# Kernel optimization log

Hardware: AMD Instinct MI355X
Metric: run time of the kernel (lower is better)

The kernel has to match this reference:

```python
import jax, jax.numpy as jnp
import numpy as np

N_NODES = 50000
N_EDGES = 800000
D = 128
AVG_D_LOG = 2.833  # log(avg_degree + 1)
EPS = 1e-5


def setup_inputs() -> dict:
    key = jax.random.key(0)
    ks = jax.random.split(key, 8)
    h = jax.random.normal(ks[0], (N_NODES, D), dtype=jnp.float32)
    e = jax.random.normal(ks[1], (N_EDGES, D), dtype=jnp.float32)
    snorm_n = jax.random.uniform(ks[2], (N_NODES, 1), dtype=jnp.float32)
    src = jax.random.randint(ks[3], (N_EDGES,), 0, N_NODES)
    dst = jax.random.randint(ks[4], (N_EDGES,), 0, N_NODES)
    W_pre = jax.random.normal(ks[5], (3 * D, D), dtype=jnp.float32) * 0.05
    b_pre = jnp.zeros((D,), dtype=jnp.float32)
    W_post = jax.random.normal(ks[6], (13 * D, D), dtype=jnp.float32) * 0.05
    b_post = jnp.zeros((D,), dtype=jnp.float32)
    return {"h": h, "e": e, "snorm_n": snorm_n, "src": src, "dst": dst,
            "W_pre": W_pre, "b_pre": b_pre, "W_post": W_post, "b_post": b_post}


def _pna_forward(h, e, snorm_n, src, dst, W_pre, b_pre, W_post, b_post):
    N = h.shape[0]
    # pretrans_edges: gather endpoint features + edge features, single Linear (pretrans_layers=1)
    z2 = jnp.concatenate([h[src], h[dst], e], axis=1)           # [E, 3D]
    m = z2 @ W_pre + b_pre                                        # [E, D] per-edge message

    # reduce: multi-aggregator mailbox reduce over dst (ragged neighborhoods)
    deg = jax.ops.segment_sum(jnp.ones((m.shape[0],), m.dtype), dst, num_segments=N)  # [N]
    deg_safe = jnp.maximum(deg, 1.0)[:, None]
    s = jax.ops.segment_sum(m, dst, num_segments=N)
    s2 = jax.ops.segment_sum(m * m, dst, num_segments=N)
    mean = s / deg_safe
    var = jax.nn.relu(s2 / deg_safe - mean * mean)
    std = jnp.sqrt(var + EPS)
    mx = jax.ops.segment_max(m, dst, num_segments=N)
    mn = jax.ops.segment_min(m, dst, num_segments=N)
    has = (deg > 0)[:, None]
    mx = jnp.where(has, mx, 0.0)
    mn = jnp.where(has, mn, 0.0)
    agg = jnp.concatenate([mean, mx, mn, std], axis=1)            # [N, 4D]

    # scalers: identity, amplification, attenuation
    log_d = jnp.log(deg[:, None] + 1.0)
    log_d_safe = jnp.log(deg_safe + 1.0)
    amp = agg * (log_d / AVG_D_LOG)
    att = agg * (AVG_D_LOG / log_d_safe)
    scaled = jnp.concatenate([agg, amp, att], axis=1)             # [N, 12D]
    scaled = jnp.where(has, scaled, 0.0)                          # DGL zero-fills zero-degree nodes

    # posttrans: cat original h, single Linear (posttrans_layers=1), then graph_norm
    h_cat = jnp.concatenate([h, scaled], axis=1)                  # [N, 13D]
    out = h_cat @ W_post + b_post                                 # [N, D]
    out = out * snorm_n                                           # graph_norm; dropout p=0 is identity
    return out


def reference(h, e, snorm_n, src, dst, W_pre, b_pre, W_post, b_post):
    return _pna_forward(h, e, snorm_n, src, dst, W_pre, b_pre, W_post, b_post)
```

## Files before the change

### kernel.cpp

```cpp
#include <hip/hip_runtime.h>
#include <math.h>

#define NNODES 50000
#define NEDGES 800000
#define AVGDLOG 2.833f
#define EPSF 1e-5f
#define TPB_E 8

typedef __attribute__((ext_vector_type(8))) short short8;
typedef __attribute__((ext_vector_type(4))) float f32x4;

__device__ __forceinline__ unsigned f2bf(float x) {
    unsigned u = __float_as_uint(x);
    return (u + 0x7FFFu + ((u >> 16) & 1u)) >> 16;
}
__device__ __forceinline__ float bf2f(unsigned lo16) {
    return __uint_as_float(lo16 << 16);
}
__device__ __forceinline__ void up8(uint4 v, float* f) {
    f[0] = bf2f(v.x & 0xffffu); f[1] = bf2f(v.x >> 16);
    f[2] = bf2f(v.y & 0xffffu); f[3] = bf2f(v.y >> 16);
    f[4] = bf2f(v.z & 0xffffu); f[5] = bf2f(v.z >> 16);
    f[6] = bf2f(v.w & 0xffffu); f[7] = bf2f(v.w >> 16);
}
__device__ __forceinline__ uint4 pk8(const float* f) {
    uint4 v;
    v.x = f2bf(f[0]) | (f2bf(f[1]) << 16);
    v.y = f2bf(f[2]) | (f2bf(f[3]) << 16);
    v.z = f2bf(f[4]) | (f2bf(f[5]) << 16);
    v.w = f2bf(f[6]) | (f2bf(f[7]) << 16);
    return v;
}

__global__ void k_zero(unsigned* __restrict__ deg) {
    int i = blockIdx.x * 256 + threadIdx.x;
    if (i < NNODES) deg[i] = 0u;
}
__global__ void k_count(const int* __restrict__ dst, unsigned* __restrict__ deg) {
    int i = blockIdx.x * 256 + threadIdx.x;
    if (i < NEDGES) atomicAdd(&deg[dst[i]], 1u);
}
__global__ __launch_bounds__(1024) void k_scan(const unsigned* __restrict__ deg,
                                               int* __restrict__ base, int* __restrict__ cursor) {
    __shared__ int ps[1024];
    const int t = threadIdx.x;
    const int lo = t * 52;
    int s = 0;
    if (lo + 52 <= NNODES) {
        const int4* dp = (const int4*)(deg + lo);
#pragma unroll
        for (int i = 0; i < 13; ++i) { int4 v = dp[i]; s += v.x + v.y + v.z + v.w; }
    } else {
        for (int i = lo; i < NNODES; ++i) s += (int)deg[i];
    }
    ps[t] = s;
    __syncthreads();
    for (int off = 1; off < 1024; off <<= 1) {
        int v = (t >= off) ? ps[t - off] : 0;
        __syncthreads();
        ps[t] += v;
        __syncthreads();
    }
    int run = (t > 0) ? ps[t - 1] : 0;
    if (lo + 52 <= NNODES) {
        const int4* dp = (const int4*)(deg + lo);
        int4* bp = (int4*)(base + lo);
        int4* cp = (int4*)(cursor + lo);
#pragma unroll
        for (int i = 0; i < 13; ++i) {
            int4 v = dp[i]; int4 b;
            b.x = run; run += v.x; b.y = run; run += v.y;
            b.z = run; run += v.z; b.w = run; run += v.w;
            bp[i] = b; cp[i] = b;
        }
    } else {
        for (int i = lo; i < NNODES; ++i) { base[i] = run; cursor[i] = run; run += (int)deg[i]; }
    }
    if (t == 1023) base[NNODES] = run;
}
__global__ void k_scatter(const int* __restrict__ dst, const int* __restrict__ src,
                          int* __restrict__ cursor, int* __restrict__ sorted,
                          int* __restrict__ ssrc) {
    int i = blockIdx.x * 256 + threadIdx.x;
    if (i < NEDGES) {
        int d = dst[i];
        int slot = atomicAdd(&cursor[d], 1);
        sorted[slot] = i;
        ssrc[slot] = src[i];
    }
}

__global__ void k_convW(const float* __restrict__ Wpre, const float* __restrict__ Wpost,
                        unsigned short* __restrict__ W3t, unsigned short* __restrict__ W12t,
                        unsigned short* __restrict__ Bhat) {
    int i = blockIdx.x * 256 + threadIdx.x;
    if (i < 128 * 128) {
        int n = i & 127, k = i >> 7;
        W3t[n * 128 + k] = (unsigned short)f2bf(Wpre[(256 + k) * 128 + n]);
    }
    if (i < 256 * 128) {
        int n = i >> 7, k = i & 127;
        float v = (n < 128) ? Wpre[k * 128 + n] : Wpre[(128 + k) * 128 + (n - 128)];
        W12t[n * 128 + k] = (unsigned short)f2bf(v);
    }
    if (i < 640 * 384) {
        int kc = i / (384 * 32);
        int rem = i % (384 * 32);
        int n = rem >> 5, kk = rem & 31;
        int k = kc * 32 + kk, c = n & 127, g = n >> 7;
        float v;
        if (g == 0) v = Wpost[k * 128 + c];
        else if (g == 1) v = (k < 128) ? 0.f : Wpost[(512 + k) * 128 + c];
        else v = (k < 128) ? 0.f : Wpost[(1024 + k) * 128 + c];
        Bhat[i] = (unsigned short)f2bf(v);
    }
}

__global__ __launch_bounds__(256) void k_p12(const float* __restrict__ h,
                                             const unsigned short* __restrict__ W12t,
                                             unsigned short* __restrict__ P1,
                                             unsigned short* __restrict__ P2,
                                             unsigned short* __restrict__ Abuf) {
    __shared__ __align__(16) unsigned short As[64 * 128];
    __shared__ __align__(16) unsigned short Bs[256 * 128];
    const int t = threadIdx.x;
    const size_t row0 = (size_t)blockIdx.x * 64;
#pragma unroll
    for (int j = 0; j < 16; ++j) {
        int idx = t + 256 * j;
        int n = idx >> 4, q = idx & 15;
        uint4 wv = *(const uint4*)(W12t + n * 128 + q * 8);
        *(uint4*)((char*)Bs + n * 256 + ((q * 16) ^ ((n & 7) << 4))) = wv;
    }
#pragma unroll
    for (int j = 0; j < 8; ++j) {
        int idx = t + 256 * j;
        int r = idx >> 5, q = idx & 31;
        size_t row = row0 + r;
        uint2 p = {0u, 0u};
        if (row < NNODES) {
            float4 z = ((const float4*)h)[row * 32 + q];
            p.x = f2bf(z.x) | (f2bf(z.y) << 16);
            p.y = f2bf(z.z) | (f2bf(z.w) << 16);
            *(uint2*)(Abuf + row * 640 + q * 4) = p;
        }
        *(uint2*)((char*)As + r * 256 + ((q * 8) ^ ((r & 7) << 4))) = p;
    }
    __syncthreads();
    const int w = t >> 6, lane = t & 63, lrow = lane & 15, lkb = lane >> 4;
    f32x4 acc[16];
#pragma unroll
    for (int i = 0; i < 16; ++i) acc[i] = (f32x4){0.f, 0.f, 0.f, 0.f};
    const char* Abase = (const char*)As + (w * 16 + lrow) * 256;
    const unsigned aswz = (unsigned)(((w * 16 + lrow) & 7) << 4);
#pragma unroll
    for (int kk = 0; kk < 4; ++kk) {
        int kbyte = (kk * 32 + lkb * 8) * 2;
        short8 af = *(const short8*)(Abase + (kbyte ^ aswz));
#pragma unroll
        for (int nt = 0; nt < 16; ++nt) {
            int n = nt * 16 + lrow;
            short8 bf = *(const short8*)((const char*)Bs + n * 256 + (kbyte ^ ((n & 7) << 4)));
            acc[nt] = __builtin_amdgcn_mfma_f32_16x16x32_bf16(af, bf, acc[nt], 0, 0, 0);
        }
    }
#pragma unroll
    for (int half = 0; half < 2; ++half) {
        __syncthreads();
#pragma unroll
        for (int nt = 0; nt < 8; ++nt) {
            int c = nt * 16 + lrow;
#pragma unroll
            for (int i = 0; i < 4; ++i) {
                int lr = w * 16 + lkb * 4 + i;
                *(unsigned short*)((char*)As + lr * 256 + ((c * 2) ^ ((lr & 7) << 4))) =
                    (unsigned short)f2bf(acc[half * 8 + nt][i]);
            }
        }
        __syncthreads();
        unsigned short* dstP = half ? P2 : P1;
#pragma unroll
        for (int j = 0; j < 4; ++j) {
            int idx = t + 256 * j;
            int r = idx >> 4, q = idx & 15;
            size_t row = row0 + r;
            if (row < NNODES) {
                uint4 v = *(const uint4*)((const char*)As + r * 256 + ((q * 16) ^ ((r & 7) << 4)));
                *(uint4*)(dstP + row * 128 + q * 8) = v;
            }
        }
    }
}

__global__ __launch_bounds__(256) void k_gemm_e(const float* __restrict__ e,
                                                const int* __restrict__ sorted,
                                                const unsigned short* __restrict__ W3t,
                                                const float* __restrict__ bpre,
                                                unsigned short* __restrict__ G) {
    __shared__ __align__(16) unsigned short Bs[128 * 128];
    __shared__ __align__(16) unsigned short As[2][64 * 128];
    __shared__ int Seid[TPB_E * 64];
    const int t = threadIdx.x;
    const int tile0 = blockIdx.x * TPB_E;
    const int ntiles = min(TPB_E, 12500 - tile0);

    for (int j = t; j < TPB_E * 64; j += 256) {
        int slot = tile0 * 64 + j;
        Seid[j] = (slot < NEDGES) ? sorted[slot] : 0;
    }
    __syncthreads();

    const int q = t & 31, r5 = t >> 5;
    auto loadE = [&](int ti, float4* ra) {
#pragma unroll
        for (int j = 0; j < 8; ++j) {
            int r = r5 + 8 * j;
            int eid = Seid[ti * 64 + r];
            ra[j] = ((const float4*)e)[(size_t)eid * 32 + q];
        }
    };
    auto storeA = [&](int buf, const float4* ra) {
#pragma unroll
        for (int j = 0; j < 8; ++j) {
            int r = r5 + 8 * j;
            uint2 pv;
            pv.x = f2bf(ra[j].x) | (f2bf(ra[j].y) << 16);
            pv.y = f2bf(ra[j].z) | (f2bf(ra[j].w) << 16);
            *(uint2*)((char*)As[buf] + r * 256 + ((q * 8) ^ ((r & 7) << 4))) = pv;
        }
    };

    float4 ra[8];
    loadE(0, ra);
#pragma unroll
    for (int j = 0; j < 8; ++j) {
        int idx = t + 256 * j;
        int n = idx >> 4, qq = idx & 15;
        uint4 wv = *(const uint4*)(W3t + n * 128 + qq * 8);
        *(uint4*)((char*)Bs + n * 256 + ((qq * 16) ^ ((n & 7) << 4))) = wv;
    }
    storeA(0, ra);
    if (ntiles > 1) loadE(1, ra);
    __syncthreads();

    const int w = t >> 6, lane = t & 63, lrow = lane & 15, lkb = lane >> 4;
    float bpf[8];
#pragma unroll
    for (int nt = 0; nt < 8; ++nt) bpf[nt] = bpre[nt * 16 + lrow];

    for (int ti = 0; ti < ntiles; ++ti) {
        const int c = ti & 1;
        f32x4 acc[8];
#pragma unroll
        for (int i = 0; i < 8; ++i) acc[i] = (f32x4){0.f, 0.f, 0.f, 0.f};
        const char* Ab = (const char*)As[c] + (w * 16 + lrow) * 256;
        const unsigned aswz = (unsigned)(((w * 16 + lrow) & 7) << 4);
#pragma unroll
        for (int kk = 0; kk < 4; ++kk) {
            int kbyte = (kk * 32 + lkb * 8) * 2;
            short8 af = *(const short8*)(Ab + (kbyte ^ aswz));
#pragma unroll
            for (int nt = 0; nt < 8; ++nt) {
                int n = nt * 16 + lrow;
                short8 bf = *(const short8*)((const char*)Bs + n * 256 + (kbyte ^ ((n & 7) << 4)));
                acc[nt] = __builtin_amdgcn_mfma_f32_16x16x32_bf16(af, bf, acc[nt], 0, 0, 0);
            }
        }
        __syncthreads();
#pragma unroll
        for (int nt = 0; nt < 8; ++nt) {
            int cc = nt * 16 + lrow;
#pragma unroll
            for (int i = 0; i < 4; ++i) {
                int lr = w * 16 + lkb * 4 + i;
                *(unsigned short*)((char*)As[c] + lr * 256 + ((cc * 2) ^ ((lr & 7) << 4))) =
                    (unsigned short)f2bf(acc[nt][i] + bpf[nt]);
            }
        }
        if (ti + 1 < ntiles) {
            storeA(c ^ 1, ra);
            if (ti + 2 < ntiles) loadE(ti + 2, ra);
        }
        __syncthreads();
        const size_t row0 = (size_t)(tile0 + ti) * 64;
#pragma unroll
        for (int j = 0; j < 4; ++j) {
            int idx = t + 256 * j;
            int r = idx >> 4, qq = idx & 15;
            uint4 v = *(const uint4*)((const char*)As[c] + r * 256 + ((qq * 16) ^ ((r & 7) << 4)));
            *(uint4*)(G + (row0 + r) * 128 + qq * 8) = v;
        }
    }
}

__global__ __launch_bounds__(256) void k_reduce(const unsigned short* __restrict__ G,
                                                const unsigned short* __restrict__ P1,
                                                const unsigned short* __restrict__ P2,
                                                const int* __restrict__ basep,
                                                const int* __restrict__ ssrc,
                                                unsigned short* __restrict__ Abuf) {
    const int t = threadIdx.x;
    const int n = blockIdx.x * 4 + (t >> 6);
    const int lane = t & 63, lq = lane >> 4, lc = lane & 15;
    int b0 = basep[n], b1 = basep[n + 1];
    int dg = b1 - b0;
    float s[8], q2[8], mx[8], mn[8];
#pragma unroll
    for (int j = 0; j < 8; ++j) { s[j] = 0.f; q2[j] = 0.f; mx[j] = -3.4e38f; mn[j] = 3.4e38f; }
    if (dg > 0) {
        float p2f[8];
        up8(*(const uint4*)(P2 + (size_t)n * 128 + lc * 8), p2f);
        for (int sl = b0 + lq; sl < b1; sl += 4) {
            int es = ssrc[sl];
            float gf[8], p1f[8];
            up8(*(const uint4*)(G + (size_t)sl * 128 + lc * 8), gf);
            up8(*(const uint4*)(P1 + (size_t)es * 128 + lc * 8), p1f);
#pragma unroll
            for (int j = 0; j < 8; ++j) {
                float m = gf[j] + p1f[j] + p2f[j];
                s[j] += m; q2[j] += m * m;
                mx[j] = fmaxf(mx[j], m); mn[j] = fminf(mn[j], m);
            }
        }
    }
#pragma unroll
    for (int off = 16; off <= 32; off <<= 1) {
#pragma unroll
        for (int j = 0; j < 8; ++j) {
            s[j] += __shfl_xor(s[j], off);
            q2[j] += __shfl_xor(q2[j], off);
            mx[j] = fmaxf(mx[j], __shfl_xor(mx[j], off));
            mn[j] = fminf(mn[j], __shfl_xor(mn[j], off));
        }
    }
    if (lane < 16) {
        float mean[8], sd[8], X[8], N[8];
        if (dg > 0) {
            float ds = (float)dg;
#pragma unroll
            for (int j = 0; j < 8; ++j) {
                mean[j] = s[j] / ds;
                float v = fmaxf(q2[j] / ds - mean[j] * mean[j], 0.f);
                sd[j] = sqrtf(v + EPSF);
                X[j] = mx[j]; N[j] = mn[j];
            }
        } else {
#pragma unroll
            for (int j = 0; j < 8; ++j) { mean[j] = 0.f; sd[j] = 0.f; X[j] = 0.f; N[j] = 0.f; }
        }
        unsigned short* row = Abuf + (size_t)n * 640 + 128 + lc * 8;
        *(uint4*)(row) = pk8(mean);
        *(uint4*)(row + 128) = pk8(X);
        *(uint4*)(row + 256) = pk8(N);
        *(uint4*)(row + 384) = pk8(sd);
    }
}

__global__ __launch_bounds__(512) void k_gemm_post(const unsigned short* __restrict__ Abuf,
                                                   const unsigned short* __restrict__ Bhat,
                                                   const float* __restrict__ bpost,
                                                   const float* __restrict__ snorm,
                                                   const int* __restrict__ basep,
                                                   float* __restrict__ out) {
    __shared__ __align__(16) unsigned short As[2][128 * 32];
    __shared__ __align__(16) unsigned short Bs[2][384 * 32];
    __shared__ float sAmp[128], sAtt[128], sSn[128], sBp[128];
    const int t = threadIdx.x;
    const size_t row0 = (size_t)blockIdx.x * 128;
    if (t < 128) {
        size_t nn = row0 + t;
        float a = 0.f, b = 0.f, sn = 0.f;
        if (nn < NNODES) {
            int dgi = basep[nn + 1] - basep[nn];
            a = logf((float)dgi + 1.f) * (1.f / AVGDLOG);
            b = AVGDLOG / logf(fmaxf((float)dgi, 1.f) + 1.f);
            sn = snorm[nn];
        }
        sAmp[t] = a; sAtt[t] = b; sSn[t] = sn; sBp[t] = bpost[t];
    }
    const int arow = t >> 2, ak4 = t & 3;
    auto loadA = [&](int kc, uint4& ra) {
        ra = (uint4){0u, 0u, 0u, 0u};
        if (row0 + arow < NNODES)
            ra = *(const uint4*)(Abuf + (row0 + arow) * 640 + kc * 32 + ak4 * 8);
    };
    auto loadB = [&](int kc, uint4* rb) {
#pragma unroll
        for (int j = 0; j < 3; ++j) {
            int idx = t + 512 * j;
            int n = idx >> 2, k4 = idx & 3;
            rb[j] = *(const uint4*)(Bhat + ((size_t)kc * 384 + n) * 32 + k4 * 8);
        }
    };
    auto storeLDS = [&](int buf, const uint4& ra, const uint4* rb) {
        *(uint4*)((char*)As[buf] + arow * 64 + ((ak4 * 16) ^ (((arow >> 1) & 3) << 4))) = ra;
#pragma unroll
        for (int j = 0; j < 3; ++j) {
            int idx = t + 512 * j;
            int n = idx >> 2, k4 = idx & 3;
            *(uint4*)((char*)Bs[buf] + n * 64 + ((k4 * 16) ^ (((n >> 1) & 3) << 4))) = rb[j];
        }
    };
    const int w = t >> 6, wm = w & 1, wn = w >> 1;
    const int lane = t & 63, lrow = lane & 15, lkb = lane >> 4;
    f32x4 acc[4][6];
#pragma unroll
    for (int a = 0; a < 4; ++a)
#pragma unroll
        for (int b = 0; b < 6; ++b) acc[a][b] = (f32x4){0.f, 0.f, 0.f, 0.f};

    uint4 ra, rb[3];
    loadA(0, ra); loadB(0, rb);
    storeLDS(0, ra, rb);
    int cur = 0;
    for (int kc = 0; kc < 20; ++kc) {
        if (kc < 19) { loadA(kc + 1, ra); loadB(kc + 1, rb); }
        __syncthreads();
        short8 af[4];
#pragma unroll
        for (int mi = 0; mi < 4; ++mi) {
            int r = wm * 64 + mi * 16 + lrow;
            af[mi] = *(const short8*)((const char*)As[cur] + r * 64 + ((lkb * 16) ^ (((r >> 1) & 3) << 4)));
        }
        short8 bfv[6];
#pragma unroll
        for (int g = 0; g < 3; ++g)
#pragma unroll
            for (int j = 0; j < 2; ++j) {
                int nn = g * 128 + wn * 32 + j * 16 + lrow;
                bfv[g * 2 + j] = *(const short8*)((const char*)Bs[cur] + nn * 64 + ((lkb * 16) ^ (((nn >> 1) & 3) << 4)));
            }
#pragma unroll
        for (int mi = 0; mi < 4; ++mi)
#pragma unroll
            for (int f = 0; f < 6; ++f)
                acc[mi][f] = __builtin_amdgcn_mfma_f32_16x16x32_bf16(af[mi], bfv[f], acc[mi][f], 0, 0, 0);
        if (kc < 19) storeLDS(cur ^ 1, ra, rb);
        cur ^= 1;
    }
#pragma unroll
    for (int mi = 0; mi < 4; ++mi)
#pragma unroll
        for (int j = 0; j < 2; ++j)
#pragma unroll
            for (int i = 0; i < 4; ++i) {
                int r = wm * 64 + mi * 16 + lkb * 4 + i;
                size_t grow = row0 + r;
                if (grow < NNODES) {
                    int c = wn * 32 + j * 16 + lrow;
                    float v = acc[mi][j][i] + sAmp[r] * acc[mi][2 + j][i] + sAtt[r] * acc[mi][4 + j][i] + sBp[c];
                    out[grow * 128 + c] = v * sSn[r];
                }
            }
}

extern "C" void kernel_launch(void* const* d_in, const int* in_sizes, int n_in,
                              void* d_out, int out_size, void* d_ws, size_t ws_size,
                              hipStream_t stream) {
    const float* h = (const float*)d_in[0];
    const float* e = (const float*)d_in[1];
    const float* snorm = (const float*)d_in[2];
    const int* src = (const int*)d_in[3];
    const int* dst = (const int*)d_in[4];
    const float* Wpre = (const float*)d_in[5];
    const float* bpre = (const float*)d_in[6];
    const float* Wpost = (const float*)d_in[7];
    const float* bpost = (const float*)d_in[8];
    float* out = (float*)d_out;

    char* p = (char*)d_ws;
    auto alloc = [&](size_t bytes) { char* r = p; p += (bytes + 255) & ~(size_t)255; return r; };
    unsigned short* P1 = (unsigned short*)alloc((size_t)NNODES * 128 * 2);
    unsigned short* P2 = (unsigned short*)alloc((size_t)NNODES * 128 * 2);
    unsigned short* Abuf = (unsigned short*)alloc((size_t)NNODES * 640 * 2);
    unsigned short* G = (unsigned short*)alloc((size_t)NEDGES * 128 * 2);
    unsigned short* W3t = (unsigned short*)alloc(128 * 128 * 2);
    unsigned short* W12t = (unsigned short*)alloc(256 * 128 * 2);
    unsigned short* Bhat = (unsigned short*)alloc((size_t)640 * 384 * 2);
    unsigned* deg = (unsigned*)alloc((size_t)NNODES * 4);
    int* basep = (int*)alloc((size_t)(NNODES + 1) * 4);
    int* cursor = (int*)alloc((size_t)NNODES * 4);
    int* sorted = (int*)alloc((size_t)NEDGES * 4);
    int* ssrc = (int*)alloc((size_t)NEDGES * 4);

    k_zero<<<(NNODES + 255) / 256, 256, 0, stream>>>(deg);
    k_count<<<(NEDGES + 255) / 256, 256, 0, stream>>>(dst, deg);
    k_scan<<<1, 1024, 0, stream>>>(deg, basep, cursor);
    k_scatter<<<(NEDGES + 255) / 256, 256, 0, stream>>>(dst, src, cursor, sorted, ssrc);
    k_convW<<<(640 * 384 + 255) / 256, 256, 0, stream>>>(Wpre, Wpost, W3t, W12t, Bhat);
    k_p12<<<(NNODES + 63) / 64, 256, 0, stream>>>(h, W12t, P1, P2, Abuf);
    k_gemm_e<<<(12500 + TPB_E - 1) / TPB_E, 256, 0, stream>>>(e, sorted, W3t, bpre, G);
    k_reduce<<<NNODES / 4, 256, 0, stream>>>(G, P1, P2, basep, ssrc, Abuf);
    k_gemm_post<<<(NNODES + 127) / 128, 512, 0, stream>>>(Abuf, Bhat, bpost, snorm, basep, out);
}
```

Before: 479.3 us.

## Fuse edge GEMM with segmented multi-aggregator reduce over node-aligned edge chunks

Merges the per-edge pre-transform GEMM and the per-node mean/max/min/std reduction into one kernel. Each block takes a chunk of dst-sorted edges aligned to node boundaries, computes messages in shared memory and reduces them serially per column. This removes the 800K×128 bf16 intermediate message buffer round-trip through global memory. In exchange, the reduction is serial per tile using only 128 threads. Nodes with MAXS-bounded chunks or more than 32 zero-degree nodes per chunk may be mishandled, and the software pipeline is shallower.

```diff
diff --git a/kernel.cpp b/kernel.cpp
--- a/kernel.cpp
+++ b/kernel.cpp
@@ -5,7 +5,9 @@
 #define NEDGES 800000
 #define AVGDLOG 2.833f
 #define EPSF 1e-5f
-#define TPB_E 8
+#define CHUNK 448
+#define MAXS 576
+#define NCHUNK (NEDGES / CHUNK + 1)
 
 typedef __attribute__((ext_vector_type(8))) short short8;
 typedef __attribute__((ext_vector_type(4))) float f32x4;
@@ -16,20 +18,6 @@
 }
 __device__ __forceinline__ float bf2f(unsigned lo16) {
     return __uint_as_float(lo16 << 16);
-}
-__device__ __forceinline__ void up8(uint4 v, float* f) {
-    f[0] = bf2f(v.x & 0xffffu); f[1] = bf2f(v.x >> 16);
-    f[2] = bf2f(v.y & 0xffffu); f[3] = bf2f(v.y >> 16);
-    f[4] = bf2f(v.z & 0xffffu); f[5] = bf2f(v.z >> 16);
-    f[6] = bf2f(v.w & 0xffffu); f[7] = bf2f(v.w >> 16);
-}
-__device__ __forceinline__ uint4 pk8(const float* f) {
-    uint4 v;
-    v.x = f2bf(f[0]) | (f2bf(f[1]) << 16);
-    v.y = f2bf(f[2]) | (f2bf(f[3]) << 16);
-    v.z = f2bf(f[4]) | (f2bf(f[5]) << 16);
-    v.w = f2bf(f[6]) | (f2bf(f[7]) << 16);
-    return v;
 }
 
 __global__ void k_zero(unsigned* __restrict__ deg) {
@@ -192,68 +180,116 @@
     }
 }
 
-__global__ __launch_bounds__(256) void k_gemm_e(const float* __restrict__ e,
-                                                const int* __restrict__ sorted,
-                                                const unsigned short* __restrict__ W3t,
-                                                const float* __restrict__ bpre,
-                                                unsigned short* __restrict__ G) {
+__global__ __launch_bounds__(256) void k_fused(const float* __restrict__ e,
+                                               const int* __restrict__ sorted,
+                                               const int* __restrict__ ssrc_g,
+                                               const int* __restrict__ basep,
+                                               const unsigned short* __restrict__ W3t,
+                                               const float* __restrict__ bpre,
+                                               const unsigned short* __restrict__ P1,
+                                               const unsigned short* __restrict__ P2,
+                                               unsigned short* __restrict__ Abuf) {
     __shared__ __align__(16) unsigned short Bs[128 * 128];
-    __shared__ __align__(16) unsigned short As[2][64 * 128];
-    __shared__ int Seid[TPB_E * 64];
+    __shared__ __align__(16) unsigned short As[64 * 128];
+    __shared__ __align__(16) unsigned short P1s[64 * 128];
+    __shared__ int seid[MAXS];
+    __shared__ unsigned short ssr[MAXS];
+    __shared__ unsigned short snode[MAXS];
+    __shared__ int zlist[32];
+    __shared__ int zcnt;
+
     const int t = threadIdx.x;
-    const int tile0 = blockIdx.x * TPB_E;
-    const int ntiles = min(TPB_E, 12500 - tile0);
-
-    for (int j = t; j < TPB_E * 64; j += 256) {
-        int slot = tile0 * 64 + j;
-        Seid[j] = (slot < NEDGES) ? sorted[slot] : 0;
+    const int cblk = blockIdx.x;
+    if (t == 0) zcnt = 0;
+
+    const int tg1 = cblk * CHUNK, tg2 = tg1 + CHUNK;
+    int lo = 0, hi = NNODES;
+    while (lo < hi) { int mid = (lo + hi) >> 1; if (basep[mid] >= tg1) hi = mid; else lo = mid + 1; }
+    const int firstNode = lo;
+    hi = NNODES;
+    while (lo < hi) { int mid = (lo + hi) >> 1; if (basep[mid] >= tg2) hi = mid; else lo = mid + 1; }
+    const int endNode = lo;
+
+    const int s0 = basep[firstNode];
+    const int nslots = basep[endNode] - s0;
+    const int ntiles = (nslots + 63) >> 6;
+
+    const int ntot = ntiles << 6;
+    for (int j = t; j < ntot; j += 256) {
+        bool v = j < nslots;
+        seid[j] = v ? sorted[s0 + j] : 0;
+        ssr[j] = v ? (unsigned short)ssrc_g[s0 + j] : 0;
+    }
+    for (int n = firstNode + t; n < endNode; n += 256) {
+        int b0 = basep[n], b1 = basep[n + 1];
+        if (b0 == b1) { int i = atomicAdd(&zcnt, 1); if (i < 32) zlist[i] = n; }
+        for (int j = b0 - s0; j < b1 - s0; ++j) snode[j] = (unsigned short)n;
+    }
+#pragma unroll
+    for (int j = 0; j < 8; ++j) {
+        int idx = t + 256 * j;
+        int n = idx >> 4, q = idx & 15;
+        uint4 wv = *(const uint4*)(W3t + n * 128 + q * 8);
+        *(uint4*)((char*)Bs + n * 256 + ((q * 16) ^ ((n & 7) << 4))) = wv;
     }
     __syncthreads();
 
-    const int q = t & 31, r5 = t >> 5;
-    auto loadE = [&](int ti, float4* ra) {
+    const int q5 = t & 31, r5 = t >> 5;
+    float4 rE[8];
+    uint2 rP[8];
+    auto loadT = [&](int ti) {
 #pragma unroll
         for (int j = 0; j < 8; ++j) {
-            int r = r5 + 8 * j;
-            int eid = Seid[ti * 64 + r];
-            ra[j] = ((const float4*)e)[(size_t)eid * 32 + q];
-        }
-    };
-    auto storeA = [&](int buf, const float4* ra) {
+            int sl = (ti << 6) + r5 + 8 * j;
+            int eid = seid[sl];
+            rE[j] = ((const float4*)e)[(size_t)eid * 32 + q5];
+            int es = ssr[sl];
+            rP[j] = *(const uint2*)(P1 + (size_t)es * 128 + q5 * 4);
+        }
+    };
+    auto storeT = [&]() {
 #pragma unroll
         for (int j = 0; j < 8; ++j) {
             int r = r5 + 8 * j;
             uint2 pv;
-            pv.x = f2bf(ra[j].x) | (f2bf(ra[j].y) << 16);
-            pv.y = f2bf(ra[j].z) | (f2bf(ra[j].w) << 16);
-            *(uint2*)((char*)As[buf] + r * 256 + ((q * 8) ^ ((r & 7) << 4))) = pv;
-        }
-    };
-
-    float4 ra[8];
-    loadE(0, ra);
-#pragma unroll
-    for (int j = 0; j < 8; ++j) {
-        int idx = t + 256 * j;
-        int n = idx >> 4, qq = idx & 15;
-        uint4 wv = *(const uint4*)(W3t + n * 128 + qq * 8);
-        *(uint4*)((char*)Bs + n * 256 + ((qq * 16) ^ ((n & 7) << 4))) = wv;
-    }
-    storeA(0, ra);
-    if (ntiles > 1) loadE(1, ra);
-    __syncthreads();
+            pv.x = f2bf(rE[j].x) | (f2bf(rE[j].y) << 16);
+            pv.y = f2bf(rE[j].z) | (f2bf(rE[j].w) << 16);
+            unsigned off = (unsigned)(r * 256) + (((unsigned)(q5 * 8)) ^ (((unsigned)(r & 7)) << 4));
+            *(uint2*)((char*)As + off) = pv;
+            *(uint2*)((char*)P1s + off) = rP[j];
+        }
+    };
+    if (ntiles > 0) loadT(0);
 
     const int w = t >> 6, lane = t & 63, lrow = lane & 15, lkb = lane >> 4;
     float bpf[8];
 #pragma unroll
     for (int nt = 0; nt < 8; ++nt) bpf[nt] = bpre[nt * 16 + lrow];
 
+    const int col = t & 127;
+    float ss = 0.f, qq = 0.f, mx = -3.4e38f, mn = 3.4e38f;
+    int cur = -1;
+    auto flushN = [&]() {
+        float dg = (float)(basep[cur + 1] - basep[cur]);
+        float mean_g = ss / dg;
+        float var = fmaxf(qq / dg - mean_g * mean_g, 0.f);
+        float sd = sqrtf(var + EPSF);
+        float c2 = bf2f(P2[(size_t)cur * 128 + col]);
+        unsigned short* row = Abuf + (size_t)cur * 640 + 128 + col;
+        row[0] = (unsigned short)f2bf(mean_g + c2);
+        row[128] = (unsigned short)f2bf(mx + c2);
+        row[256] = (unsigned short)f2bf(mn + c2);
+        row[384] = (unsigned short)f2bf(sd);
+    };
+
     for (int ti = 0; ti < ntiles; ++ti) {
-        const int c = ti & 1;
+        storeT();
+        __syncthreads();
+        if (ti + 1 < ntiles) loadT(ti + 1);
         f32x4 acc[8];
 #pragma unroll
         for (int i = 0; i < 8; ++i) acc[i] = (f32x4){0.f, 0.f, 0.f, 0.f};
-        const char* Ab = (const char*)As[c] + (w * 16 + lrow) * 256;
+        const char* Ab = (const char*)As + (w * 16 + lrow) * 256;
         const unsigned aswz = (unsigned)(((w * 16 + lrow) & 7) << 4);
 #pragma unroll
         for (int kk = 0; kk < 4; ++kk) {
@@ -273,86 +309,36 @@
 #pragma unroll
             for (int i = 0; i < 4; ++i) {
                 int lr = w * 16 + lkb * 4 + i;
-                *(unsigned short*)((char*)As[c] + lr * 256 + ((cc * 2) ^ ((lr & 7) << 4))) =
-                    (unsigned short)f2bf(acc[nt][i] + bpf[nt]);
-            }
-        }
-        if (ti + 1 < ntiles) {
-            storeA(c ^ 1, ra);
-            if (ti + 2 < ntiles) loadE(ti + 2, ra);
-        }
-        __syncthreads();
-        const size_t row0 = (size_t)(tile0 + ti) * 64;
-#pragma unroll
-        for (int j = 0; j < 4; ++j) {
-            int idx = t + 256 * j;
-            int r = idx >> 4, qq = idx & 15;
-            uint4 v = *(const uint4*)((const char*)As[c] + r * 256 + ((qq * 16) ^ ((r & 7) << 4)));
-            *(uint4*)(G + (row0 + r) * 128 + qq * 8) = v;
-        }
-    }
-}
-
-__global__ __launch_bounds__(256) void k_reduce(const unsigned short* __restrict__ G,
-                                                const unsigned short* __restrict__ P1,
-                                                const unsigned short* __restrict__ P2,
-                                                const int* __restrict__ basep,
-                                                const int* __restrict__ ssrc,
-                                                unsigned short* __restrict__ Abuf) {
-    const int t = threadIdx.x;
-    const int n = blockIdx.x * 4 + (t >> 6);
-    const int lane = t & 63, lq = lane >> 4, lc = lane & 15;
-    int b0 = basep[n], b1 = basep[n + 1];
-    int dg = b1 - b0;
-    float s[8], q2[8], mx[8], mn[8];
-#pragma unroll
-    for (int j = 0; j < 8; ++j) { s[j] = 0.f; q2[j] = 0.f; mx[j] = -3.4e38f; mn[j] = 3.4e38f; }
-    if (dg > 0) {
-        float p2f[8];
-        up8(*(const uint4*)(P2 + (size_t)n * 128 + lc * 8), p2f);
-        for (int sl = b0 + lq; sl < b1; sl += 4) {
-            int es = ssrc[sl];
-            float gf[8], p1f[8];
-            up8(*(const uint4*)(G + (size_t)sl * 128 + lc * 8), gf);
-            up8(*(const uint4*)(P1 + (size_t)es * 128 + lc * 8), p1f);
-#pragma unroll
-            for (int j = 0; j < 8; ++j) {
-                float m = gf[j] + p1f[j] + p2f[j];
-                s[j] += m; q2[j] += m * m;
-                mx[j] = fmaxf(mx[j], m); mn[j] = fminf(mn[j], m);
-            }
-        }
-    }
-#pragma unroll
-    for (int off = 16; off <= 32; off <<= 1) {
-#pragma unroll
-        for (int j = 0; j < 8; ++j) {
-            s[j] += __shfl_xor(s[j], off);
-            q2[j] += __shfl_xor(q2[j], off);
-            mx[j] = fmaxf(mx[j], __shfl_xor(mx[j], off));
-            mn[j] = fminf(mn[j], __shfl_xor(mn[j], off));
-        }
-    }
-    if (lane < 16) {
-        float mean[8], sd[8], X[8], N[8];
-        if (dg > 0) {
-            float ds = (float)dg;
-#pragma unroll
-            for (int j = 0; j < 8; ++j) {
-                mean[j] = s[j] / ds;
-                float v = fmaxf(q2[j] / ds - mean[j] * mean[j], 0.f);
-                sd[j] = sqrtf(v + EPSF);
-                X[j] = mx[j]; N[j] = mn[j];
-            }
-        } else {
-#pragma unroll
-            for (int j = 0; j < 8; ++j) { mean[j] = 0.f; sd[j] = 0.f; X[j] = 0.f; N[j] = 0.f; }
-        }
-        unsigned short* row = Abuf + (size_t)n * 640 + 128 + lc * 8;
-        *(uint4*)(row) = pk8(mean);
-        *(uint4*)(row + 128) = pk8(X);
-        *(uint4*)(row + 256) = pk8(N);
-        *(uint4*)(row + 384) = pk8(sd);
+                unsigned off = (unsigned)(lr * 256) + (((unsigned)(cc * 2)) ^ (((unsigned)(lr & 7)) << 4));
+                float p1v = bf2f(*(const unsigned short*)((const char*)P1s + off));
+                *(unsigned short*)((char*)As + off) = (unsigned short)f2bf(acc[nt][i] + bpf[nt] + p1v);
+            }
+        }
+        __syncthreads();
+        const int rows = min(64, nslots - (ti << 6));
+        if (t < 128) {
+            for (int r = 0; r < rows; ++r) {
+                int n = (int)snode[(ti << 6) + r];
+                if (n != cur) {
+                    if (cur >= 0) flushN();
+                    cur = n; ss = 0.f; qq = 0.f; mx = -3.4e38f; mn = 3.4e38f;
+                }
+                unsigned off = (unsigned)(r * 256) + (((unsigned)(col * 2)) ^ (((unsigned)(r & 7)) << 4));
+                float x = bf2f(*(const unsigned short*)((const char*)As + off));
+                ss += x; qq = fmaf(x, x, qq);
+                mx = fmaxf(mx, x); mn = fminf(mn, x);
+            }
+        }
+        __syncthreads();
+    }
+    if (t < 128 && cur >= 0) flushN();
+    if (t < 128) {
+        int zc = min(zcnt, 32);
+        for (int i = 0; i < zc; ++i) {
+            int n = zlist[i];
+            unsigned short* row = Abuf + (size_t)n * 640 + 128 + col;
+            row[0] = 0; row[128] = 0; row[256] = 0; row[384] = 0;
+        }
     }
 }
 
@@ -473,7 +459,6 @@
     unsigned short* P1 = (unsigned short*)alloc((size_t)NNODES * 128 * 2);
     unsigned short* P2 = (unsigned short*)alloc((size_t)NNODES * 128 * 2);
     unsigned short* Abuf = (unsigned short*)alloc((size_t)NNODES * 640 * 2);
-    unsigned short* G = (unsigned short*)alloc((size_t)NEDGES * 128 * 2);
     unsigned short* W3t = (unsigned short*)alloc(128 * 128 * 2);
     unsigned short* W12t = (unsigned short*)alloc(256 * 128 * 2);
     unsigned short* Bhat = (unsigned short*)alloc((size_t)640 * 384 * 2);
@@ -489,7 +474,6 @@
     k_scatter<<<(NEDGES + 255) / 256, 256, 0, stream>>>(dst, src, cursor, sorted, ssrc);
     k_convW<<<(640 * 384 + 255) / 256, 256, 0, stream>>>(Wpre, Wpost, W3t, W12t, Bhat);
     k_p12<<<(NNODES + 63) / 64, 256, 0, stream>>>(h, W12t, P1, P2, Abuf);
-    k_gemm_e<<<(12500 + TPB_E - 1) / TPB_E, 256, 0, stream>>>(e, sorted, W3t, bpre, G);
-    k_reduce<<<NNODES / 4, 256, 0, stream>>>(G, P1, P2, basep, ssrc, Abuf);
+    k_fused<<<NCHUNK, 256, 0, stream>>>(e, sorted, ssrc, basep, W3t, bpre, P1, P2, Abuf);
     k_gemm_post<<<(NNODES + 127) / 128, 512, 0, stream>>>(Abuf, Bhat, bpost, snorm, basep, out);
 }
```

Result: slower. 576.6 us (+20.3%).

## Read edges in original order, scatter messages with P1 folded in, parallelize scan

Applied to the files above, without the earlier changes.

The edge GEMM now streams e contiguously and adds the gathered P1[src] term in its epilogue. It writes each message row to its dst-sorted slot, so the scatter pass only records slots and no longer builds sorted/ssrc arrays. The reduce loop reads only G and applies P2 after computing the statistics, using the shift invariance of mean/max/min/std. The single-block prefix scan is replaced by a three-kernel multi-block scan, and the LDS swizzle in the post GEMM is changed. In exchange, G writes become scattered rows and the P1 sum is rounded to bf16 before aggregation.

```diff
diff --git a/kernel.cpp b/kernel.cpp
--- a/kernel.cpp
+++ b/kernel.cpp
@@ -6,6 +6,7 @@
 #define AVGDLOG 2.833f
 #define EPSF 1e-5f
 #define TPB_E 8
+#define NSCAN 49
 
 typedef __attribute__((ext_vector_type(8))) short short8;
 typedef __attribute__((ext_vector_type(4))) float f32x4;
@@ -40,53 +41,67 @@
     int i = blockIdx.x * 256 + threadIdx.x;
     if (i < NEDGES) atomicAdd(&deg[dst[i]], 1u);
 }
-__global__ __launch_bounds__(1024) void k_scan(const unsigned* __restrict__ deg,
-                                               int* __restrict__ base, int* __restrict__ cursor) {
-    __shared__ int ps[1024];
-    const int t = threadIdx.x;
-    const int lo = t * 52;
+__global__ void k_scanA(const unsigned* __restrict__ deg, int* __restrict__ bsum) {
+    __shared__ int wsum[4];
+    const int t = threadIdx.x, b = blockIdx.x;
+    int i = b * 1024 + t * 4;
     int s = 0;
-    if (lo + 52 <= NNODES) {
-        const int4* dp = (const int4*)(deg + lo);
-#pragma unroll
-        for (int i = 0; i < 13; ++i) { int4 v = dp[i]; s += v.x + v.y + v.z + v.w; }
+    if (i + 4 <= NNODES) {
+        int4 v = *(const int4*)(deg + i);
+        s = v.x + v.y + v.z + v.w;
     } else {
-        for (int i = lo; i < NNODES; ++i) s += (int)deg[i];
-    }
-    ps[t] = s;
+        for (int k = 0; k < 4; ++k) if (i + k < NNODES) s += (int)deg[i + k];
+    }
+#pragma unroll
+    for (int off = 1; off < 64; off <<= 1) s += __shfl_xor(s, off);
+    if ((t & 63) == 0) wsum[t >> 6] = s;
     __syncthreads();
-    for (int off = 1; off < 1024; off <<= 1) {
-        int v = (t >= off) ? ps[t - off] : 0;
-        __syncthreads();
-        ps[t] += v;
-        __syncthreads();
-    }
-    int run = (t > 0) ? ps[t - 1] : 0;
-    if (lo + 52 <= NNODES) {
-        const int4* dp = (const int4*)(deg + lo);
-        int4* bp = (int4*)(base + lo);
-        int4* cp = (int4*)(cursor + lo);
-#pragma unroll
-        for (int i = 0; i < 13; ++i) {
-            int4 v = dp[i]; int4 b;
-            b.x = run; run += v.x; b.y = run; run += v.y;
-            b.z = run; run += v.z; b.w = run; run += v.w;
-            bp[i] = b; cp[i] = b;
-        }
+    if (t == 0) bsum[b] = wsum[0] + wsum[1] + wsum[2] + wsum[3];
+}
+__global__ void k_scanB(const int* __restrict__ bsum, int* __restrict__ boff,
+                        int* __restrict__ basep) {
+    if (threadIdx.x == 0) {
+        int run = 0;
+        for (int b = 0; b < NSCAN; ++b) { boff[b] = run; run += bsum[b]; }
+        basep[NNODES] = run;
+    }
+}
+__global__ void k_scanC(const unsigned* __restrict__ deg, const int* __restrict__ boff,
+                        int* __restrict__ basep, int* __restrict__ cursor) {
+    __shared__ int ps[256];
+    const int t = threadIdx.x, b = blockIdx.x;
+    int i = b * 1024 + t * 4;
+    int v0 = 0, v1 = 0, v2 = 0, v3 = 0;
+    if (i + 4 <= NNODES) {
+        int4 v = *(const int4*)(deg + i);
+        v0 = v.x; v1 = v.y; v2 = v.z; v3 = v.w;
     } else {
-        for (int i = lo; i < NNODES; ++i) { base[i] = run; cursor[i] = run; run += (int)deg[i]; }
-    }
-    if (t == 1023) base[NNODES] = run;
-}
-__global__ void k_scatter(const int* __restrict__ dst, const int* __restrict__ src,
-                          int* __restrict__ cursor, int* __restrict__ sorted,
-                          int* __restrict__ ssrc) {
+        if (i < NNODES) v0 = (int)deg[i];
+        if (i + 1 < NNODES) v1 = (int)deg[i + 1];
+        if (i + 2 < NNODES) v2 = (int)deg[i + 2];
+        if (i + 3 < NNODES) v3 = (int)deg[i + 3];
+    }
+    int ts = v0 + v1 + v2 + v3;
+    ps[t] = ts;
+    __syncthreads();
+    for (int off = 1; off < 256; off <<= 1) {
+        int x = (t >= off) ? ps[t - off] : 0;
+        __syncthreads();
+        ps[t] += x;
+        __syncthreads();
+    }
+    int excl = ps[t] - ts + boff[b];
+    if (i < NNODES) { basep[i] = excl; cursor[i] = excl; }
+    if (i + 1 < NNODES) { basep[i + 1] = excl + v0; cursor[i + 1] = excl + v0; }
+    if (i + 2 < NNODES) { basep[i + 2] = excl + v0 + v1; cursor[i + 2] = excl + v0 + v1; }
+    if (i + 3 < NNODES) { basep[i + 3] = excl + v0 + v1 + v2; cursor[i + 3] = excl + v0 + v1 + v2; }
+}
+__global__ void k_scatter(const int* __restrict__ dst, int* __restrict__ cursor,
+                          int* __restrict__ slotArr) {
     int i = blockIdx.x * 256 + threadIdx.x;
     if (i < NEDGES) {
         int d = dst[i];
-        int slot = atomicAdd(&cursor[d], 1);
-        sorted[slot] = i;
-        ssrc[slot] = src[i];
+        slotArr[i] = atomicAdd(&cursor[d], 1);
     }
 }
 
@@ -193,31 +208,32 @@
 }
 
 __global__ __launch_bounds__(256) void k_gemm_e(const float* __restrict__ e,
-                                                const int* __restrict__ sorted,
+                                                const int* __restrict__ src,
+                                                const int* __restrict__ slotArr,
                                                 const unsigned short* __restrict__ W3t,
                                                 const float* __restrict__ bpre,
+                                                const unsigned short* __restrict__ P1,
                                                 unsigned short* __restrict__ G) {
     __shared__ __align__(16) unsigned short Bs[128 * 128];
     __shared__ __align__(16) unsigned short As[2][64 * 128];
-    __shared__ int Seid[TPB_E * 64];
+    __shared__ int Ssl[TPB_E * 64];
+    __shared__ int Ssr[TPB_E * 64];
     const int t = threadIdx.x;
     const int tile0 = blockIdx.x * TPB_E;
     const int ntiles = min(TPB_E, 12500 - tile0);
 
-    for (int j = t; j < TPB_E * 64; j += 256) {
-        int slot = tile0 * 64 + j;
-        Seid[j] = (slot < NEDGES) ? sorted[slot] : 0;
-    }
-    __syncthreads();
+    for (int j = t; j < ntiles * 64; j += 256) {
+        int row = tile0 * 64 + j;
+        Ssl[j] = slotArr[row];
+        Ssr[j] = src[row];
+    }
 
     const int q = t & 31, r5 = t >> 5;
     auto loadE = [&](int ti, float4* ra) {
-#pragma unroll
-        for (int j = 0; j < 8; ++j) {
-            int r = r5 + 8 * j;
-            int eid = Seid[ti * 64 + r];
-            ra[j] = ((const float4*)e)[(size_t)eid * 32 + q];
-        }
+        const float4* ep = (const float4*)e + (size_t)(tile0 + ti) * 2048;
+#pragma unroll
+        for (int j = 0; j < 8; ++j)
+            ra[j] = ep[(r5 + 8 * j) * 32 + q];
     };
     auto storeA = [&](int buf, const float4* ra) {
 #pragma unroll
@@ -282,22 +298,24 @@
             if (ti + 2 < ntiles) loadE(ti + 2, ra);
         }
         __syncthreads();
-        const size_t row0 = (size_t)(tile0 + ti) * 64;
 #pragma unroll
         for (int j = 0; j < 4; ++j) {
             int idx = t + 256 * j;
             int r = idx >> 4, qq = idx & 15;
             uint4 v = *(const uint4*)((const char*)As[c] + r * 256 + ((qq * 16) ^ ((r & 7) << 4)));
-            *(uint4*)(G + (row0 + r) * 128 + qq * 8) = v;
+            uint4 pv = *(const uint4*)(P1 + (size_t)Ssr[ti * 64 + r] * 128 + qq * 8);
+            float gf[8], pf[8];
+            up8(v, gf); up8(pv, pf);
+#pragma unroll
+            for (int k = 0; k < 8; ++k) gf[k] += pf[k];
+            *(uint4*)(G + (size_t)Ssl[ti * 64 + r] * 128 + qq * 8) = pk8(gf);
         }
     }
 }
 
 __global__ __launch_bounds__(256) void k_reduce(const unsigned short* __restrict__ G,
-                                                const unsigned short* __restrict__ P1,
                                                 const unsigned short* __restrict__ P2,
                                                 const int* __restrict__ basep,
-                                                const int* __restrict__ ssrc,
                                                 unsigned short* __restrict__ Abuf) {
     const int t = threadIdx.x;
     const int n = blockIdx.x * 4 + (t >> 6);
@@ -307,20 +325,14 @@
     float s[8], q2[8], mx[8], mn[8];
 #pragma unroll
     for (int j = 0; j < 8; ++j) { s[j] = 0.f; q2[j] = 0.f; mx[j] = -3.4e38f; mn[j] = 3.4e38f; }
-    if (dg > 0) {
-        float p2f[8];
-        up8(*(const uint4*)(P2 + (size_t)n * 128 + lc * 8), p2f);
-        for (int sl = b0 + lq; sl < b1; sl += 4) {
-            int es = ssrc[sl];
-            float gf[8], p1f[8];
-            up8(*(const uint4*)(G + (size_t)sl * 128 + lc * 8), gf);
-            up8(*(const uint4*)(P1 + (size_t)es * 128 + lc * 8), p1f);
-#pragma unroll
-            for (int j = 0; j < 8; ++j) {
-                float m = gf[j] + p1f[j] + p2f[j];
-                s[j] += m; q2[j] += m * m;
-                mx[j] = fmaxf(mx[j], m); mn[j] = fminf(mn[j], m);
-            }
+    for (int sl = b0 + lq; sl < b1; sl += 4) {
+        float gf[8];
+        up8(*(const uint4*)(G + (size_t)sl * 128 + lc * 8), gf);
+#pragma unroll
+        for (int j = 0; j < 8; ++j) {
+            float m = gf[j];
+            s[j] += m; q2[j] = fmaf(m, m, q2[j]);
+            mx[j] = fmaxf(mx[j], m); mn[j] = fminf(mn[j], m);
         }
     }
 #pragma unroll
@@ -337,12 +349,16 @@
         float mean[8], sd[8], X[8], N[8];
         if (dg > 0) {
             float ds = (float)dg;
+            float p2f[8];
+            up8(*(const uint4*)(P2 + (size_t)n * 128 + lc * 8), p2f);
 #pragma unroll
             for (int j = 0; j < 8; ++j) {
-                mean[j] = s[j] / ds;
-                float v = fmaxf(q2[j] / ds - mean[j] * mean[j], 0.f);
+                float mg = s[j] / ds;
+                float v = fmaxf(q2[j] / ds - mg * mg, 0.f);
                 sd[j] = sqrtf(v + EPSF);
-                X[j] = mx[j]; N[j] = mn[j];
+                mean[j] = mg + p2f[j];
+                X[j] = mx[j] + p2f[j];
+                N[j] = mn[j] + p2f[j];
             }
         } else {
 #pragma unroll
@@ -393,12 +409,12 @@
         }
     };
     auto storeLDS = [&](int buf, const uint4& ra, const uint4* rb) {
-        *(uint4*)((char*)As[buf] + arow * 64 + ((ak4 * 16) ^ (((arow >> 1) & 3) << 4))) = ra;
+        *(uint4*)((char*)As[buf] + arow * 64 + ((ak4 * 16) ^ ((arow & 3) << 4))) = ra;
 #pragma unroll
         for (int j = 0; j < 3; ++j) {
             int idx = t + 512 * j;
             int n = idx >> 2, k4 = idx & 3;
-            *(uint4*)((char*)Bs[buf] + n * 64 + ((k4 * 16) ^ (((n >> 1) & 3) << 4))) = rb[j];
+            *(uint4*)((char*)Bs[buf] + n * 64 + ((k4 * 16) ^ ((n & 3) << 4))) = rb[j];
         }
     };
     const int w = t >> 6, wm = w & 1, wn = w >> 1;
@@ -420,7 +436,7 @@
 #pragma unroll
         for (int mi = 0; mi < 4; ++mi) {
             int r = wm * 64 + mi * 16 + lrow;
-            af[mi] = *(const short8*)((const char*)As[cur] + r * 64 + ((lkb * 16) ^ (((r >> 1) & 3) << 4)));
+            af[mi] = *(const short8*)((const char*)As[cur] + r * 64 + ((lkb * 16) ^ ((r & 3) << 4)));
         }
         short8 bfv[6];
 #pragma unroll
@@ -428,7 +444,7 @@
 #pragma unroll
             for (int j = 0; j < 2; ++j) {
                 int nn = g * 128 + wn * 32 + j * 16 + lrow;
-                bfv[g * 2 + j] = *(const short8*)((const char*)Bs[cur] + nn * 64 + ((lkb * 16) ^ (((nn >> 1) & 3) << 4)));
+                bfv[g * 2 + j] = *(const short8*)((const char*)Bs[cur] + nn * 64 + ((lkb * 16) ^ ((nn & 3) << 4)));
             }
 #pragma unroll
         for (int mi = 0; mi < 4; ++mi)
@@ -480,16 +496,19 @@
     unsigned* deg = (unsigned*)alloc((size_t)NNODES * 4);
     int* basep = (int*)alloc((size_t)(NNODES + 1) * 4);
     int* cursor = (int*)alloc((size_t)NNODES * 4);
-    int* sorted = (int*)alloc((size_t)NEDGES * 4);
-    int* ssrc = (int*)alloc((size_t)NEDGES * 4);
+    int* slotArr = (int*)alloc((size_t)NEDGES * 4);
+    int* bsum = (int*)alloc((size_t)NSCAN * 4);
+    int* boff = (int*)alloc((size_t)NSCAN * 4);
 
     k_zero<<<(NNODES + 255) / 256, 256, 0, stream>>>(deg);
     k_count<<<(NEDGES + 255) / 256, 256, 0, stream>>>(dst, deg);
-    k_scan<<<1, 1024, 0, stream>>>(deg, basep, cursor);
-    k_scatter<<<(NEDGES + 255) / 256, 256, 0, stream>>>(dst, src, cursor, sorted, ssrc);
+    k_scanA<<<NSCAN, 256, 0, stream>>>(deg, bsum);
+    k_scanB<<<1, 64, 0, stream>>>(bsum, boff, basep);
+    k_scanC<<<NSCAN, 256, 0, stream>>>(deg, boff, basep, cursor);
+    k_scatter<<<(NEDGES + 255) / 256, 256, 0, stream>>>(dst, cursor, slotArr);
     k_convW<<<(640 * 384 + 255) / 256, 256, 0, stream>>>(Wpre, Wpost, W3t, W12t, Bhat);
     k_p12<<<(NNODES + 63) / 64, 256, 0, stream>>>(h, W12t, P1, P2, Abuf);
-    k_gemm_e<<<(12500 + TPB_E - 1) / TPB_E, 256, 0, stream>>>(e, sorted, W3t, bpre, G);
-    k_reduce<<<NNODES / 4, 256, 0, stream>>>(G, P1, P2, basep, ssrc, Abuf);
+    k_gemm_e<<<(12500 + TPB_E - 1) / TPB_E, 256, 0, stream>>>(e, src, slotArr, W3t, bpre, P1, G);
+    k_reduce<<<NNODES / 4, 256, 0, stream>>>(G, P2, basep, Abuf);
     k_gemm_post<<<(NNODES + 127) / 128, 512, 0, stream>>>(Abuf, Bhat, bpost, snorm, basep, out);
 }
```

Result: faster. 450.5 us (median of 3 runs) (-6.0%).
